# Kernel tuning notes

Hardware: AMD Instinct MI355X
Metric: run time of the kernel (lower is better)

Reference implementation:

```python
import jax, jax.numpy as jnp
import numpy as np

B, Q, K, DQ, DK, H, DV = 4, 512, 512, 512, 512, 256, 512


def setup_inputs() -> dict:
    key = jax.random.key(0)
    ks = jax.random.split(key, 9)
    return {
        "query": jax.random.normal(ks[0], (B, Q, DQ), dtype=jnp.float32),
        "key": jax.random.normal(ks[1], (B, K, DK), dtype=jnp.float32),
        "value": jax.random.normal(ks[2], (B, K, DV), dtype=jnp.float32),
        "Wq": jax.random.normal(ks[3], (DQ, H), dtype=jnp.float32) / np.sqrt(DQ),
        "bq": jax.random.normal(ks[4], (H,), dtype=jnp.float32) * 0.01,
        "Wk": jax.random.normal(ks[5], (DK, H), dtype=jnp.float32) / np.sqrt(DK),
        "bk": jax.random.normal(ks[6], (H,), dtype=jnp.float32) * 0.01,
        "wv": jax.random.normal(ks[7], (H,), dtype=jnp.float32) / np.sqrt(H),
        "bv": jax.random.normal(ks[8], (), dtype=jnp.float32) * 0.01,
    }


def reference(query, key, value, Wq, bq, Wk, bk, wv, bv):
    # Projections: [B,Q,H] and [B,K,H]
    q = jnp.einsum("bqd,dh->bqh", query, Wq) + bq
    k = jnp.einsum("bkd,dh->bkh", key, Wk) + bk
    # Broadcast add + tanh: [B,Q,K,H] (the large intermediate)
    feat = jnp.tanh(q[:, :, None, :] + k[:, None, :, :])
    # Linear-to-scalar score: [B,Q,K]
    score = jnp.einsum("bqkh,h->bqk", feat, wv) + bv
    attention_weight = jax.nn.softmax(score, axis=-1)
    # Dropout is identity at eval; weighted sum over keys: [B,Q,DV]
    context = jnp.einsum("bqk,bkd->bqd", attention_weight, value)
    return (context, attention_weight)
```

## Files before the change

kernel.cpp:

```cpp
#include <hip/hip_runtime.h>
#include <hip/hip_bf16.h>

#define B_ 4
#define Q_ 512
#define K_ 512
#define DQ_ 512
#define H_ 256
#define DV_ 512

#define SC2 2.8853900817779268f

typedef unsigned short u16;
typedef short bf16x8 __attribute__((ext_vector_type(8)));
typedef float f32x4 __attribute__((ext_vector_type(4)));
typedef float f32x2 __attribute__((ext_vector_type(2)));
typedef unsigned short u16x4 __attribute__((ext_vector_type(4)));

__device__ __forceinline__ unsigned bsplit(float a) {
    unsigned u  = __float_as_uint(a);
    unsigned hi = (u + 0x7FFFu + ((u >> 16) & 1u)) >> 16;
    float hf = __uint_as_float(hi << 16);
    float l  = a - hf;
    unsigned ul = __float_as_uint(l);
    unsigned lo = (ul + 0x7FFFu + ((ul >> 16) & 1u)) >> 16;
    return (hi << 16) | lo;
}

__device__ __forceinline__ u16 brn(float a) {
    unsigned u = __float_as_uint(a);
    return (u16)((u + 0x7FFFu + ((u >> 16) & 1u)) >> 16);
}

__device__ __forceinline__ void gld16(const void* g, void* l) {
    __builtin_amdgcn_global_load_lds(
        (const __attribute__((address_space(1))) unsigned int*)g,
        (__attribute__((address_space(3))) unsigned int*)l, 16, 0, 0);
}

__device__ __forceinline__ void pair_acc(
    f32x2 Eq0, f32x2 Eq1, float ek0, float ek1,
    float w0, float w1, float w01, f32x2& acc)
{
    f32x2 e0 = Eq0 * (f32x2){ek0, ek0};
    f32x2 e1 = Eq1 * (f32x2){ek1, ek1};
    f32x2 s  = e0 + e1;
    f32x2 den = __builtin_elementwise_fma(e0, e1, s);
    den = den + (f32x2){1.f, 1.f};
    f32x2 num = __builtin_elementwise_fma(e1, (f32x2){w0, w0}, (f32x2){w01, w01});
    num = __builtin_elementwise_fma(e0, (f32x2){w1, w1}, num);
    f32x2 r = {__builtin_amdgcn_rcpf(den.x), __builtin_amdgcn_rcpf(den.y)};
    acc = __builtin_elementwise_fma(num, r, acc);
}

__global__ __launch_bounds__(256) void prep_all(
    const float* __restrict__ query, const float* __restrict__ key,
    const float* __restrict__ Wq, const float* __restrict__ Wk,
    const float* __restrict__ value,
    u16* __restrict__ qA_hi,
    u16* __restrict__ WT_hi, u16* __restrict__ WT_lo,
    u16* __restrict__ vT_hi)
{
    const int bx  = blockIdx.x;
    const int tid = threadIdx.x;

    if (bx < 2048) {
        const int z = bx >> 10;
        const float* src = z ? key : query;
        u16* dh = qA_hi + (long long)z * 1048576;
        long long i4 = (long long)(bx & 1023) * 256 + tid;
        float4 v = ((const float4*)src)[i4];
        u16x4 h4 = {brn(v.x), brn(v.y), brn(v.z), brn(v.w)};
        *(u16x4*)(dh + i4 * 4) = h4;
        return;
    }

    __shared__ float t[32][33];
    const int flat = bx - 2048;
    const int z  = flat >> 8;
    const int rem = flat & 255;
    const int gx = rem & 15, gy = rem >> 4;
    const int x = tid & 31, y = tid >> 5;
    const float* src; u16 *dh, *dl; int C;
    if (z < 2) {
        if (gy >= 8) return;
        src = z ? Wk : Wq; C = 256;
        dh = WT_hi + (long long)z * 131072;
        dl = WT_lo + (long long)z * 131072;
    } else {
        src = value + (long long)(z - 2) * 262144; C = 512;
        dh = vT_hi + (long long)(z - 2) * 262144;
        dl = nullptr;
    }
    const int r0 = gx * 32, c0 = gy * 32;
    #pragma unroll
    for (int i = 0; i < 32; i += 8)
        t[y + i][x] = src[(long long)(r0 + y + i) * C + c0 + x];
    __syncthreads();
    {
        const int r = tid >> 3, c = tid & 7;
        long long o = (long long)(c0 + r) * 512 + r0 + 4 * c;
        if (dl) {
            unsigned p0 = bsplit(t[4 * c + 0][r]);
            unsigned p1 = bsplit(t[4 * c + 1][r]);
            unsigned p2 = bsplit(t[4 * c + 2][r]);
            unsigned p3 = bsplit(t[4 * c + 3][r]);
            u16x4 h4 = {(u16)(p0 >> 16), (u16)(p1 >> 16), (u16)(p2 >> 16), (u16)(p3 >> 16)};
            u16x4 l4 = {(u16)(p0 & 0xFFFF), (u16)(p1 & 0xFFFF), (u16)(p2 & 0xFFFF), (u16)(p3 & 0xFFFF)};
            *(u16x4*)(dh + o) = h4;
            *(u16x4*)(dl + o) = l4;
        } else {
            u16x4 h4 = {brn(t[4 * c + 0][r]), brn(t[4 * c + 1][r]),
                        brn(t[4 * c + 2][r]), brn(t[4 * c + 3][r])};
            *(u16x4*)(dh + o) = h4;
        }
    }
}

__global__ __launch_bounds__(256) void proj_gemm(
    const u16* __restrict__ Ah0,
    const u16* __restrict__ Bh0, const u16* __restrict__ Bl0,
    const float* __restrict__ biasq, const float* __restrict__ biask,
    float* __restrict__ outp,
    long long sA, long long sB, long long sO)
{
    const int z = blockIdx.z;
    const int Kd = DQ_;
    const u16* Ah = Ah0 + z * sA;
    const u16* Bh = Bh0 + z * sB;
    const u16* Bl = Bl0 + z * sB;

    const int m0 = blockIdx.x * 64;
    const int n0 = blockIdx.y * 64;

    __shared__ u16 AhS[2][64 * 64], BhS[2][64 * 64], BlS[2][64 * 64];

    const int tid = threadIdx.x;
    const int lane = tid & 63, w = tid >> 6;
    const int wr = w >> 1, wc = w & 1;
    const int lrow = lane & 15, lgrp = lane >> 4;

    f32x4 acc[2][2] = {};

    const int idx0 = tid, idx1 = tid + 256;
    const int row0 = idx0 >> 3, u0 = idx0 & 7;
    const int row1 = idx1 >> 3, u1 = idx1 & 7;
    const long long goA0 = (long long)(m0 + row0) * Kd + ((u0 ^ (row0 & 7)) << 3);
    const long long goA1 = (long long)(m0 + row1) * Kd + ((u1 ^ (row1 & 7)) << 3);
    const long long goB0 = (long long)(n0 + row0) * Kd + ((u0 ^ (row0 & 7)) << 3);
    const long long goB1 = (long long)(n0 + row1) * Kd + ((u1 ^ (row1 & 7)) << 3);

#define STAGE(BI, K0) do {                                    \
        gld16(Ah + goA0 + (K0), &AhS[BI][idx0 * 8]);          \
        gld16(Bh + goB0 + (K0), &BhS[BI][idx0 * 8]);          \
        gld16(Bl + goB0 + (K0), &BlS[BI][idx0 * 8]);          \
        gld16(Ah + goA1 + (K0), &AhS[BI][idx1 * 8]);          \
        gld16(Bh + goB1 + (K0), &BhS[BI][idx1 * 8]);          \
        gld16(Bl + goB1 + (K0), &BlS[BI][idx1 * 8]);          \
    } while (0)

    STAGE(0, 0);
    __syncthreads();

    int cur = 0;
    for (int k0 = 0; k0 < Kd; k0 += 64) {
        if (k0 + 64 < Kd) STAGE(cur ^ 1, k0 + 64);

        #pragma unroll
        for (int kk = 0; kk < 2; ++kk) {
            bf16x8 ah[2], bh[2], bl[2];
            #pragma unroll
            for (int f = 0; f < 2; ++f) {
                int ar = wr * 32 + f * 16 + lrow;
                int au = (kk * 4 + lgrp) ^ (ar & 7);
                ah[f] = *(const bf16x8*)(&AhS[cur][ar * 64 + au * 8]);
                int br = wc * 32 + f * 16 + lrow;
                int bu = (kk * 4 + lgrp) ^ (br & 7);
                bh[f] = *(const bf16x8*)(&BhS[cur][br * 64 + bu * 8]);
                bl[f] = *(const bf16x8*)(&BlS[cur][br * 64 + bu * 8]);
            }
            #pragma unroll
            for (int fm = 0; fm < 2; ++fm)
                #pragma unroll
                for (int fn = 0; fn < 2; ++fn) {
                    acc[fm][fn] = __builtin_amdgcn_mfma_f32_16x16x32_bf16(ah[fm], bh[fn], acc[fm][fn], 0, 0, 0);
                    acc[fm][fn] = __builtin_amdgcn_mfma_f32_16x16x32_bf16(ah[fm], bl[fn], acc[fm][fn], 0, 0, 0);
                }
        }
        __syncthreads();
        cur ^= 1;
    }
#undef STAGE

    const float* bs = z ? biask : biasq;
    #pragma unroll
    for (int fm = 0; fm < 2; ++fm)
        #pragma unroll
        for (int fn = 0; fn < 2; ++fn)
            #pragma unroll
            for (int r = 0; r < 4; ++r) {
                int m = m0 + wr * 32 + fm * 16 + lgrp * 4 + r;
                int n = n0 + wc * 32 + fn * 16 + lrow;
                float v = __builtin_amdgcn_exp2f((acc[fm][fn][r] + bs[n]) * SC2);
                if (z == 0) {
                    outp[(((long long)(m >> 2) * H_ + n) << 2) + (m & 3)] = v;
                } else {
                    int bb = m >> 9, k = m & 511;
                    outp[sO + (((long long)(bb * 64 + (n >> 2)) * 512 + k) << 2) + (n & 3)] = v;
                }
            }
}

__global__ __launch_bounds__(256) void pv_gemm(
    const u16* __restrict__ A0, const u16* __restrict__ B0,
    float* __restrict__ ctx)
{
    const int z = blockIdx.z;
    const int Kd = K_;
    const u16* A = A0 + (long long)z * 262144;
    const u16* Bp = B0 + (long long)z * 262144;
    float* C = ctx + (long long)z * 262144;

    const int m0 = blockIdx.x * 64;
    const int n0 = blockIdx.y * 64;

    __shared__ u16 AS[2][64 * 64], BS[2][64 * 64];

    const int tid = threadIdx.x;
    const int lane = tid & 63, w = tid >> 6;
    const int wr = w >> 1, wc = w & 1;
    const int lrow = lane & 15, lgrp = lane >> 4;

    f32x4 acc[2][2] = {};

    const int idx0 = tid, idx1 = tid + 256;
    const int row0 = idx0 >> 3, u0 = idx0 & 7;
    const int row1 = idx1 >> 3, u1 = idx1 & 7;
    const long long goA0 = (long long)(m0 + row0) * Kd + ((u0 ^ (row0 & 7)) << 3);
    const long long goA1 = (long long)(m0 + row1) * Kd + ((u1 ^ (row1 & 7)) << 3);
    const long long goB0 = (long long)(n0 + row0) * Kd + ((u0 ^ (row0 & 7)) << 3);
    const long long goB1 = (long long)(n0 + row1) * Kd + ((u1 ^ (row1 & 7)) << 3);

#define STAGE(BI, K0) do {                                    \
        gld16(A  + goA0 + (K0), &AS[BI][idx0 * 8]);           \
        gld16(Bp + goB0 + (K0), &BS[BI][idx0 * 8]);           \
        gld16(A  + goA1 + (K0), &AS[BI][idx1 * 8]);           \
        gld16(Bp + goB1 + (K0), &BS[BI][idx1 * 8]);           \
    } while (0)

    STAGE(0, 0);
    __syncthreads();

    int cur = 0;
    for (int k0 = 0; k0 < Kd; k0 += 64) {
        if (k0 + 64 < Kd) STAGE(cur ^ 1, k0 + 64);

        #pragma unroll
        for (int kk = 0; kk < 2; ++kk) {
            bf16x8 a[2], b[2];
            #pragma unroll
            for (int f = 0; f < 2; ++f) {
                int ar = wr * 32 + f * 16 + lrow;
                int au = (kk * 4 + lgrp) ^ (ar & 7);
                a[f] = *(const bf16x8*)(&AS[cur][ar * 64 + au * 8]);
                int br = wc * 32 + f * 16 + lrow;
                int bu = (kk * 4 + lgrp) ^ (br & 7);
                b[f] = *(const bf16x8*)(&BS[cur][br * 64 + bu * 8]);
            }
            #pragma unroll
            for (int fm = 0; fm < 2; ++fm)
                #pragma unroll
                for (int fn = 0; fn < 2; ++fn)
                    acc[fm][fn] = __builtin_amdgcn_mfma_f32_16x16x32_bf16(a[fm], b[fn], acc[fm][fn], 0, 0, 0);
        }
        __syncthreads();
        cur ^= 1;
    }
#undef STAGE

    #pragma unroll
    for (int fm = 0; fm < 2; ++fm)
        #pragma unroll
        for (int fn = 0; fn < 2; ++fn)
            #pragma unroll
            for (int r = 0; r < 4; ++r) {
                int m = m0 + wr * 32 + fm * 16 + lgrp * 4 + r;
                int n = n0 + wc * 32 + fn * 16 + lrow;
                C[(long long)m * DV_ + n] = acc[fm][fn][r];
            }
}

#define QT 8

__global__ __launch_bounds__(1024) void score_softmax(
    const float* __restrict__ qp4E,
    const float* __restrict__ kT4E,
    const float* __restrict__ wv,
    float* __restrict__ attn_out,
    u16* __restrict__ aB_hi)
{
    const int b   = blockIdx.y;
    const int q0  = blockIdx.x * QT;
    const int tid = threadIdx.x;
    const int k16 = tid & 255;
    const int qtr = tid >> 8;
    const int lane = tid & 63;

    __shared__ float lq[H_][8];
    __shared__ float lwp[H_ / 2][4];
    __shared__ float pacc[3][2][256][8];
    __shared__ float red[4][QT];

    if (tid < 256) {
        const float4* qA = (const float4*)qp4E + ((long long)(b * (Q_ / 4) + 2 * blockIdx.x)) * H_;
        *(float4*)&lq[tid][0] = qA[tid];
    } else if (tid < 512) {
        int h = tid - 256;
        const float4* qB = (const float4*)qp4E + ((long long)(b * (Q_ / 4) + 2 * blockIdx.x + 1)) * H_;
        *(float4*)&lq[h][4] = qB[h];
    } else if (tid < 512 + 128) {
        int p = tid - 512;
        float w0 = wv[2 * p], w1 = wv[2 * p + 1];
        lwp[p][0] = w0; lwp[p][1] = w1; lwp[p][2] = w0 + w1; lwp[p][3] = 0.f;
    }
    __syncthreads();

    f32x2 aA[4] = {{0.f,0.f},{0.f,0.f},{0.f,0.f},{0.f,0.f}};
    f32x2 aB[4] = {{0.f,0.f},{0.f,0.f},{0.f,0.f},{0.f,0.f}};
    const float4* kvec = (const float4*)kT4E + (long long)b * (H_ / 4) * K_ + k16;
    const int g0 = qtr * 16;

    float4 kA = kvec[(long long)g0 * K_];
    float4 kB = kvec[(long long)g0 * K_ + 256];
    #pragma unroll 2
    for (int gi = 0; gi < 16; ++gi) {
        const int g = g0 + gi;
        float4 kAc = kA, kBc = kB;
        if (gi < 15) {
            kA = kvec[(long long)(g + 1) * K_];
            kB = kvec[(long long)(g + 1) * K_ + 256];
        }
        float4 wp0 = *(const float4*)&lwp[(g << 1) + 0][0];
        float4 wp1 = *(const float4*)&lwp[(g << 1) + 1][0];

        float4 qa0 = *(const float4*)&lq[(g << 2) + 0][0];
        float4 qb0 = *(const float4*)&lq[(g << 2) + 0][4];
        float4 qa1 = *(const float4*)&lq[(g << 2) + 1][0];
        float4 qb1 = *(const float4*)&lq[(g << 2) + 1][4];
        float4 qa2 = *(const float4*)&lq[(g << 2) + 2][0];
        float4 qb2 = *(const float4*)&lq[(g << 2) + 2][4];
        float4 qa3 = *(const float4*)&lq[(g << 2) + 3][0];
        float4 qb3 = *(const float4*)&lq[(g << 2) + 3][4];

        f32x2 q0p[4] = {{qa0.x,qa0.y},{qa0.z,qa0.w},{qb0.x,qb0.y},{qb0.z,qb0.w}};
        f32x2 q1p[4] = {{qa1.x,qa1.y},{qa1.z,qa1.w},{qb1.x,qb1.y},{qb1.z,qb1.w}};
        f32x2 q2p[4] = {{qa2.x,qa2.y},{qa2.z,qa2.w},{qb2.x,qb2.y},{qb2.z,qb2.w}};
        f32x2 q3p[4] = {{qa3.x,qa3.y},{qa3.z,qa3.w},{qb3.x,qb3.y},{qb3.z,qb3.w}};

        #pragma unroll
        for (int qp = 0; qp < 4; ++qp) {
            pair_acc(q0p[qp], q1p[qp], kAc.x, kAc.y, wp0.x, wp0.y, wp0.z, aA[qp]);
            pair_acc(q2p[qp], q3p[qp], kAc.z, kAc.w, wp1.x, wp1.y, wp1.z, aA[qp]);
            pair_acc(q0p[qp], q1p[qp], kBc.x, kBc.y, wp0.x, wp0.y, wp0.z, aB[qp]);
            pair_acc(q2p[qp], q3p[qp], kBc.z, kBc.w, wp1.x, wp1.y, wp1.z, aB[qp]);
        }
    }

    if (qtr) {
        float4 vA0 = make_float4(aA[0].x, aA[0].y, aA[1].x, aA[1].y);
        float4 vA1 = make_float4(aA[2].x, aA[2].y, aA[3].x, aA[3].y);
        float4 vB0 = make_float4(aB[0].x, aB[0].y, aB[1].x, aB[1].y);
        float4 vB1 = make_float4(aB[2].x, aB[2].y, aB[3].x, aB[3].y);
        *(float4*)&pacc[qtr - 1][0][k16][0] = vA0;
        *(float4*)&pacc[qtr - 1][0][k16][4] = vA1;
        *(float4*)&pacc[qtr - 1][1][k16][0] = vB0;
        *(float4*)&pacc[qtr - 1][1][k16][4] = vB1;
    }
    __syncthreads();

    float e[2][QT];
    if (!qtr) {
        float s[2][QT];
        #pragma unroll
        for (int qp = 0; qp < 4; ++qp) {
            s[0][2*qp]   = aA[qp].x;
            s[0][2*qp+1] = aA[qp].y;
            s[1][2*qp]   = aB[qp].x;
            s[1][2*qp+1] = aB[qp].y;
        }
        #pragma unroll
        for (int o = 0; o < 3; ++o) {
            #pragma unroll
            for (int kk = 0; kk < 2; ++kk) {
                float4 t0 = *(const float4*)&pacc[o][kk][k16][0];
                float4 t1 = *(const float4*)&pacc[o][kk][k16][4];
                s[kk][0] += t0.x; s[kk][1] += t0.y; s[kk][2] += t0.z; s[kk][3] += t0.w;
                s[kk][4] += t1.x; s[kk][5] += t1.y; s[kk][6] += t1.z; s[kk][7] += t1.w;
            }
        }
        #pragma unroll
        for (int kk = 0; kk < 2; ++kk)
            #pragma unroll
            for (int qq = 0; qq < QT; ++qq)
                e[kk][qq] = __builtin_amdgcn_exp2f(-SC2 * s[kk][qq]);
        #pragma unroll
        for (int qq = 0; qq < QT; ++qq) {
            float v = e[0][qq] + e[1][qq];
            #pragma unroll
            for (int off = 32; off; off >>= 1) v += __shfl_xor(v, off);
            if (lane == 0) red[tid >> 6][qq] = v;
        }
    }
    __syncthreads();
    if (!qtr) {
        #pragma unroll
        for (int qq = 0; qq < QT; ++qq) {
            float v = red[0][qq] + red[1][qq] + red[2][qq] + red[3][qq];
            float rv = __builtin_amdgcn_rcpf(v);
            #pragma unroll
            for (int kk = 0; kk < 2; ++kk) {
                float a = e[kk][qq] * rv;
                long long o = (long long)(b * Q_ + q0 + qq) * K_ + k16 + kk * 256;
                attn_out[o] = a;
                aB_hi[o] = brn(a);
            }
        }
    }
}

extern "C" void kernel_launch(void* const* d_in, const int* in_sizes, int n_in,
                              void* d_out, int out_size, void* d_ws, size_t ws_size,
                              hipStream_t stream) {
    const float* query = (const float*)d_in[0];
    const float* key   = (const float*)d_in[1];
    const float* value = (const float*)d_in[2];
    const float* Wq    = (const float*)d_in[3];
    const float* bq    = (const float*)d_in[4];
    const float* Wk    = (const float*)d_in[5];
    const float* bk    = (const float*)d_in[6];
    const float* wv    = (const float*)d_in[7];

    float* out = (float*)d_out;
    float* ctx_out  = out;
    float* attn_out = out + (size_t)B_ * Q_ * DV_;

    float* ws   = (float*)d_ws;
    float* qp4  = ws;
    float* kT4  = qp4 + 524288;
    u16* qA_hi  = (u16*)(kT4 + 524288);
    u16* WqT_hi = qA_hi + 2097152;
    u16* WqT_lo = WqT_hi + 262144;
    u16* vT_hi  = WqT_lo + 262144;
    u16* aB_hi  = vT_hi + 1048576;
    (void)n_in; (void)ws_size; (void)in_sizes; (void)out_size;

    hipLaunchKernelGGL(prep_all, dim3(3584), dim3(256), 0, stream,
                       query, key, Wq, Wk, value,
                       qA_hi, WqT_hi, WqT_lo, vT_hi);

    hipLaunchKernelGGL(proj_gemm, dim3(32, 4, 2), dim3(256), 0, stream,
                       qA_hi, WqT_hi, WqT_lo, bq, bk, qp4,
                       (long long)1048576, (long long)131072, (long long)524288);

    hipLaunchKernelGGL(score_softmax, dim3(Q_ / QT, B_), dim3(1024), 0, stream,
                       qp4, kT4, wv, attn_out, aB_hi);

    hipLaunchKernelGGL(pv_gemm, dim3(8, 8, 4), dim3(256), 0, stream,
                       aB_hi, vT_hi, ctx_out);
}
```

Before: 60.33 us.

## Fuse all four stages into one persistent kernel with grid barriers

Replaces the four separate launches (prep, projection GEMM, score/softmax, PV GEMM) with a single 256-block persistent kernel of 1024 threads. The stages are separated by software grid-wide barriers built on atomic counters, and a memset clears the counters before launch. This removes per-launch overhead and the drain and fill gaps between kernels. In exchange the tiling changes to one 16x16 MFMA tile per wave with 1024-thread blocks, which may lower per-stage efficiency. The spin barriers also depend on all 256 blocks being resident at once, otherwise the kernel deadlocks.

```diff
diff --git a/kernel.cpp b/kernel.cpp
--- a/kernel.cpp
+++ b/kernel.cpp
@@ -52,377 +52,353 @@
     acc = __builtin_elementwise_fma(num, r, acc);
 }
 
-__global__ __launch_bounds__(256) void prep_all(
-    const float* __restrict__ query, const float* __restrict__ key,
-    const float* __restrict__ Wq, const float* __restrict__ Wk,
-    const float* __restrict__ value,
-    u16* __restrict__ qA_hi,
-    u16* __restrict__ WT_hi, u16* __restrict__ WT_lo,
-    u16* __restrict__ vT_hi)
-{
-    const int bx  = blockIdx.x;
-    const int tid = threadIdx.x;
-
-    if (bx < 2048) {
-        const int z = bx >> 10;
-        const float* src = z ? key : query;
-        u16* dh = qA_hi + (long long)z * 1048576;
-        long long i4 = (long long)(bx & 1023) * 256 + tid;
-        float4 v = ((const float4*)src)[i4];
-        u16x4 h4 = {brn(v.x), brn(v.y), brn(v.z), brn(v.w)};
-        *(u16x4*)(dh + i4 * 4) = h4;
-        return;
-    }
-
-    __shared__ float t[32][33];
-    const int flat = bx - 2048;
-    const int z  = flat >> 8;
-    const int rem = flat & 255;
-    const int gx = rem & 15, gy = rem >> 4;
-    const int x = tid & 31, y = tid >> 5;
-    const float* src; u16 *dh, *dl; int C;
-    if (z < 2) {
-        if (gy >= 8) return;
-        src = z ? Wk : Wq; C = 256;
-        dh = WT_hi + (long long)z * 131072;
-        dl = WT_lo + (long long)z * 131072;
-    } else {
-        src = value + (long long)(z - 2) * 262144; C = 512;
-        dh = vT_hi + (long long)(z - 2) * 262144;
-        dl = nullptr;
-    }
-    const int r0 = gx * 32, c0 = gy * 32;
-    #pragma unroll
-    for (int i = 0; i < 32; i += 8)
-        t[y + i][x] = src[(long long)(r0 + y + i) * C + c0 + x];
+__device__ __forceinline__ void gsync(unsigned* syncp, int slot) {
     __syncthreads();
-    {
-        const int r = tid >> 3, c = tid & 7;
-        long long o = (long long)(c0 + r) * 512 + r0 + 4 * c;
-        if (dl) {
-            unsigned p0 = bsplit(t[4 * c + 0][r]);
-            unsigned p1 = bsplit(t[4 * c + 1][r]);
-            unsigned p2 = bsplit(t[4 * c + 2][r]);
-            unsigned p3 = bsplit(t[4 * c + 3][r]);
-            u16x4 h4 = {(u16)(p0 >> 16), (u16)(p1 >> 16), (u16)(p2 >> 16), (u16)(p3 >> 16)};
-            u16x4 l4 = {(u16)(p0 & 0xFFFF), (u16)(p1 & 0xFFFF), (u16)(p2 & 0xFFFF), (u16)(p3 & 0xFFFF)};
-            *(u16x4*)(dh + o) = h4;
-            *(u16x4*)(dl + o) = l4;
+    if (threadIdx.x == 0) {
+        unsigned* cnt  = syncp + slot * 32;
+        unsigned* flag = syncp + slot * 32 + 16;
+        __threadfence();
+        unsigned prev = atomicAdd(cnt, 1u);
+        if (prev == gridDim.x - 1) {
+            atomicExch(flag, 1u);
         } else {
-            u16x4 h4 = {brn(t[4 * c + 0][r]), brn(t[4 * c + 1][r]),
-                        brn(t[4 * c + 2][r]), brn(t[4 * c + 3][r])};
-            *(u16x4*)(dh + o) = h4;
-        }
-    }
-}
-
-__global__ __launch_bounds__(256) void proj_gemm(
-    const u16* __restrict__ Ah0,
-    const u16* __restrict__ Bh0, const u16* __restrict__ Bl0,
-    const float* __restrict__ biasq, const float* __restrict__ biask,
-    float* __restrict__ outp,
-    long long sA, long long sB, long long sO)
-{
-    const int z = blockIdx.z;
-    const int Kd = DQ_;
-    const u16* Ah = Ah0 + z * sA;
-    const u16* Bh = Bh0 + z * sB;
-    const u16* Bl = Bl0 + z * sB;
-
-    const int m0 = blockIdx.x * 64;
-    const int n0 = blockIdx.y * 64;
-
-    __shared__ u16 AhS[2][64 * 64], BhS[2][64 * 64], BlS[2][64 * 64];
-
-    const int tid = threadIdx.x;
-    const int lane = tid & 63, w = tid >> 6;
-    const int wr = w >> 1, wc = w & 1;
-    const int lrow = lane & 15, lgrp = lane >> 4;
-
-    f32x4 acc[2][2] = {};
-
-    const int idx0 = tid, idx1 = tid + 256;
-    const int row0 = idx0 >> 3, u0 = idx0 & 7;
-    const int row1 = idx1 >> 3, u1 = idx1 & 7;
-    const long long goA0 = (long long)(m0 + row0) * Kd + ((u0 ^ (row0 & 7)) << 3);
-    const long long goA1 = (long long)(m0 + row1) * Kd + ((u1 ^ (row1 & 7)) << 3);
-    const long long goB0 = (long long)(n0 + row0) * Kd + ((u0 ^ (row0 & 7)) << 3);
-    const long long goB1 = (long long)(n0 + row1) * Kd + ((u1 ^ (row1 & 7)) << 3);
-
-#define STAGE(BI, K0) do {                                    \
-        gld16(Ah + goA0 + (K0), &AhS[BI][idx0 * 8]);          \
-        gld16(Bh + goB0 + (K0), &BhS[BI][idx0 * 8]);          \
-        gld16(Bl + goB0 + (K0), &BlS[BI][idx0 * 8]);          \
-        gld16(Ah + goA1 + (K0), &AhS[BI][idx1 * 8]);          \
-        gld16(Bh + goB1 + (K0), &BhS[BI][idx1 * 8]);          \
-        gld16(Bl + goB1 + (K0), &BlS[BI][idx1 * 8]);          \
-    } while (0)
-
-    STAGE(0, 0);
-    __syncthreads();
-
-    int cur = 0;
-    for (int k0 = 0; k0 < Kd; k0 += 64) {
-        if (k0 + 64 < Kd) STAGE(cur ^ 1, k0 + 64);
-
-        #pragma unroll
-        for (int kk = 0; kk < 2; ++kk) {
-            bf16x8 ah[2], bh[2], bl[2];
-            #pragma unroll
-            for (int f = 0; f < 2; ++f) {
-                int ar = wr * 32 + f * 16 + lrow;
-                int au = (kk * 4 + lgrp) ^ (ar & 7);
-                ah[f] = *(const bf16x8*)(&AhS[cur][ar * 64 + au * 8]);
-                int br = wc * 32 + f * 16 + lrow;
-                int bu = (kk * 4 + lgrp) ^ (br & 7);
-                bh[f] = *(const bf16x8*)(&BhS[cur][br * 64 + bu * 8]);
-                bl[f] = *(const bf16x8*)(&BlS[cur][br * 64 + bu * 8]);
-            }
-            #pragma unroll
-            for (int fm = 0; fm < 2; ++fm)
-                #pragma unroll
-                for (int fn = 0; fn < 2; ++fn) {
-                    acc[fm][fn] = __builtin_amdgcn_mfma_f32_16x16x32_bf16(ah[fm], bh[fn], acc[fm][fn], 0, 0, 0);
-                    acc[fm][fn] = __builtin_amdgcn_mfma_f32_16x16x32_bf16(ah[fm], bl[fn], acc[fm][fn], 0, 0, 0);
-                }
-        }
-        __syncthreads();
-        cur ^= 1;
-    }
-#undef STAGE
-
-    const float* bs = z ? biask : biasq;
-    #pragma unroll
-    for (int fm = 0; fm < 2; ++fm)
-        #pragma unroll
-        for (int fn = 0; fn < 2; ++fn)
-            #pragma unroll
-            for (int r = 0; r < 4; ++r) {
-                int m = m0 + wr * 32 + fm * 16 + lgrp * 4 + r;
-                int n = n0 + wc * 32 + fn * 16 + lrow;
-                float v = __builtin_amdgcn_exp2f((acc[fm][fn][r] + bs[n]) * SC2);
-                if (z == 0) {
-                    outp[(((long long)(m >> 2) * H_ + n) << 2) + (m & 3)] = v;
-                } else {
-                    int bb = m >> 9, k = m & 511;
-                    outp[sO + (((long long)(bb * 64 + (n >> 2)) * 512 + k) << 2) + (n & 3)] = v;
-                }
-            }
-}
-
-__global__ __launch_bounds__(256) void pv_gemm(
-    const u16* __restrict__ A0, const u16* __restrict__ B0,
-    float* __restrict__ ctx)
-{
-    const int z = blockIdx.z;
-    const int Kd = K_;
-    const u16* A = A0 + (long long)z * 262144;
-    const u16* Bp = B0 + (long long)z * 262144;
-    float* C = ctx + (long long)z * 262144;
-
-    const int m0 = blockIdx.x * 64;
-    const int n0 = blockIdx.y * 64;
-
-    __shared__ u16 AS[2][64 * 64], BS[2][64 * 64];
-
-    const int tid = threadIdx.x;
-    const int lane = tid & 63, w = tid >> 6;
-    const int wr = w >> 1, wc = w & 1;
-    const int lrow = lane & 15, lgrp = lane >> 4;
-
-    f32x4 acc[2][2] = {};
-
-    const int idx0 = tid, idx1 = tid + 256;
-    const int row0 = idx0 >> 3, u0 = idx0 & 7;
-    const int row1 = idx1 >> 3, u1 = idx1 & 7;
-    const long long goA0 = (long long)(m0 + row0) * Kd + ((u0 ^ (row0 & 7)) << 3);
-    const long long goA1 = (long long)(m0 + row1) * Kd + ((u1 ^ (row1 & 7)) << 3);
-    const long long goB0 = (long long)(n0 + row0) * Kd + ((u0 ^ (row0 & 7)) << 3);
-    const long long goB1 = (long long)(n0 + row1) * Kd + ((u1 ^ (row1 & 7)) << 3);
-
-#define STAGE(BI, K0) do {                                    \
-        gld16(A  + goA0 + (K0), &AS[BI][idx0 * 8]);           \
-        gld16(Bp + goB0 + (K0), &BS[BI][idx0 * 8]);           \
-        gld16(A  + goA1 + (K0), &AS[BI][idx1 * 8]);           \
-        gld16(Bp + goB1 + (K0), &BS[BI][idx1 * 8]);           \
-    } while (0)
-
-    STAGE(0, 0);
-    __syncthreads();
-
-    int cur = 0;
-    for (int k0 = 0; k0 < Kd; k0 += 64) {
-        if (k0 + 64 < Kd) STAGE(cur ^ 1, k0 + 64);
-
-        #pragma unroll
-        for (int kk = 0; kk < 2; ++kk) {
-            bf16x8 a[2], b[2];
-            #pragma unroll
-            for (int f = 0; f < 2; ++f) {
-                int ar = wr * 32 + f * 16 + lrow;
-                int au = (kk * 4 + lgrp) ^ (ar & 7);
-                a[f] = *(const bf16x8*)(&AS[cur][ar * 64 + au * 8]);
-                int br = wc * 32 + f * 16 + lrow;
-                int bu = (kk * 4 + lgrp) ^ (br & 7);
-                b[f] = *(const bf16x8*)(&BS[cur][br * 64 + bu * 8]);
-            }
-            #pragma unroll
-            for (int fm = 0; fm < 2; ++fm)
-                #pragma unroll
-                for (int fn = 0; fn < 2; ++fn)
-                    acc[fm][fn] = __builtin_amdgcn_mfma_f32_16x16x32_bf16(a[fm], b[fn], acc[fm][fn], 0, 0, 0);
-        }
-        __syncthreads();
-        cur ^= 1;
-    }
-#undef STAGE
-
-    #pragma unroll
-    for (int fm = 0; fm < 2; ++fm)
-        #pragma unroll
-        for (int fn = 0; fn < 2; ++fn)
-            #pragma unroll
-            for (int r = 0; r < 4; ++r) {
-                int m = m0 + wr * 32 + fm * 16 + lgrp * 4 + r;
-                int n = n0 + wc * 32 + fn * 16 + lrow;
-                C[(long long)m * DV_ + n] = acc[fm][fn][r];
-            }
-}
-
-#define QT 8
-
-__global__ __launch_bounds__(1024) void score_softmax(
-    const float* __restrict__ qp4E,
-    const float* __restrict__ kT4E,
-    const float* __restrict__ wv,
-    float* __restrict__ attn_out,
-    u16* __restrict__ aB_hi)
-{
-    const int b   = blockIdx.y;
-    const int q0  = blockIdx.x * QT;
-    const int tid = threadIdx.x;
-    const int k16 = tid & 255;
-    const int qtr = tid >> 8;
-    const int lane = tid & 63;
-
-    __shared__ float lq[H_][8];
-    __shared__ float lwp[H_ / 2][4];
-    __shared__ float pacc[3][2][256][8];
-    __shared__ float red[4][QT];
-
-    if (tid < 256) {
-        const float4* qA = (const float4*)qp4E + ((long long)(b * (Q_ / 4) + 2 * blockIdx.x)) * H_;
-        *(float4*)&lq[tid][0] = qA[tid];
-    } else if (tid < 512) {
-        int h = tid - 256;
-        const float4* qB = (const float4*)qp4E + ((long long)(b * (Q_ / 4) + 2 * blockIdx.x + 1)) * H_;
-        *(float4*)&lq[h][4] = qB[h];
-    } else if (tid < 512 + 128) {
-        int p = tid - 512;
-        float w0 = wv[2 * p], w1 = wv[2 * p + 1];
-        lwp[p][0] = w0; lwp[p][1] = w1; lwp[p][2] = w0 + w1; lwp[p][3] = 0.f;
+            while (atomicAdd(flag, 0u) == 0u) __builtin_amdgcn_s_sleep(2);
+        }
+        __threadfence();
     }
     __syncthreads();
-
-    f32x2 aA[4] = {{0.f,0.f},{0.f,0.f},{0.f,0.f},{0.f,0.f}};
-    f32x2 aB[4] = {{0.f,0.f},{0.f,0.f},{0.f,0.f},{0.f,0.f}};
-    const float4* kvec = (const float4*)kT4E + (long long)b * (H_ / 4) * K_ + k16;
-    const int g0 = qtr * 16;
-
-    float4 kA = kvec[(long long)g0 * K_];
-    float4 kB = kvec[(long long)g0 * K_ + 256];
-    #pragma unroll 2
-    for (int gi = 0; gi < 16; ++gi) {
-        const int g = g0 + gi;
-        float4 kAc = kA, kBc = kB;
-        if (gi < 15) {
-            kA = kvec[(long long)(g + 1) * K_];
-            kB = kvec[(long long)(g + 1) * K_ + 256];
-        }
-        float4 wp0 = *(const float4*)&lwp[(g << 1) + 0][0];
-        float4 wp1 = *(const float4*)&lwp[(g << 1) + 1][0];
-
-        float4 qa0 = *(const float4*)&lq[(g << 2) + 0][0];
-        float4 qb0 = *(const float4*)&lq[(g << 2) + 0][4];
-        float4 qa1 = *(const float4*)&lq[(g << 2) + 1][0];
-        float4 qb1 = *(const float4*)&lq[(g << 2) + 1][4];
-        float4 qa2 = *(const float4*)&lq[(g << 2) + 2][0];
-        float4 qb2 = *(const float4*)&lq[(g << 2) + 2][4];
-        float4 qa3 = *(const float4*)&lq[(g << 2) + 3][0];
-        float4 qb3 = *(const float4*)&lq[(g << 2) + 3][4];
-
-        f32x2 q0p[4] = {{qa0.x,qa0.y},{qa0.z,qa0.w},{qb0.x,qb0.y},{qb0.z,qb0.w}};
-        f32x2 q1p[4] = {{qa1.x,qa1.y},{qa1.z,qa1.w},{qb1.x,qb1.y},{qb1.z,qb1.w}};
-        f32x2 q2p[4] = {{qa2.x,qa2.y},{qa2.z,qa2.w},{qb2.x,qb2.y},{qb2.z,qb2.w}};
-        f32x2 q3p[4] = {{qa3.x,qa3.y},{qa3.z,qa3.w},{qb3.x,qb3.y},{qb3.z,qb3.w}};
-
+}
+
+#define QT 8
+
+__global__ __launch_bounds__(1024) void fused_all(
+    const float* __restrict__ query, const float* __restrict__ key,
+    const float* __restrict__ value,
+    const float* __restrict__ Wq, const float* __restrict__ bq,
+    const float* __restrict__ Wk, const float* __restrict__ bk,
+    const float* __restrict__ wv,
+    float* __restrict__ ctx_out, float* __restrict__ attn_out,
+    unsigned* __restrict__ syncp,
+    float* __restrict__ qp4E, float* __restrict__ kT4E,
+    u16* __restrict__ qA_hi, u16* __restrict__ WT_hi, u16* __restrict__ WT_lo,
+    u16* __restrict__ vT_hi, u16* __restrict__ aB_hi)
+{
+    __shared__ __align__(16) unsigned char smem[61440];
+    const int tid = threadIdx.x;
+    const int bid = blockIdx.x;
+    const int lane = tid & 63;
+    const int lrow = lane & 15, lgrp = lane >> 4;
+
+    {
+        int gid = bid * 1024 + tid;
+        float4 vq = ((const float4*)query)[gid];
+        float4 vk = ((const float4*)key)[gid];
+        u16x4 hq = {brn(vq.x), brn(vq.y), brn(vq.z), brn(vq.w)};
+        u16x4 hk = {brn(vk.x), brn(vk.y), brn(vk.z), brn(vk.w)};
+        *(u16x4*)(qA_hi + (long long)gid * 4) = hq;
+        *(u16x4*)(qA_hi + 1048576 + (long long)gid * 4) = hk;
+
+        const int grp = tid >> 8, lt = tid & 255;
+        const int x = lt & 31, y = lt >> 5;
+        float (*tg)[33] = (float(*)[33])(smem + grp * 4224);
         #pragma unroll
-        for (int qp = 0; qp < 4; ++qp) {
-            pair_acc(q0p[qp], q1p[qp], kAc.x, kAc.y, wp0.x, wp0.y, wp0.z, aA[qp]);
-            pair_acc(q2p[qp], q3p[qp], kAc.z, kAc.w, wp1.x, wp1.y, wp1.z, aA[qp]);
-            pair_acc(q0p[qp], q1p[qp], kBc.x, kBc.y, wp0.x, wp0.y, wp0.z, aB[qp]);
-            pair_acc(q2p[qp], q3p[qp], kBc.z, kBc.w, wp1.x, wp1.y, wp1.z, aB[qp]);
+        for (int rnd = 0; rnd < 2; ++rnd) {
+            int tidc = bid * 8 + grp * 2 + rnd;
+            bool act = tidc < 1280;
+            const float* src = query; u16 *dh = nullptr, *dl = nullptr;
+            int C = 512, r0 = 0, c0 = 0;
+            if (act) {
+                int z, gx, gy;
+                if (tidc < 256) {
+                    z = tidc >> 7; int r2 = tidc & 127; gx = r2 & 15; gy = r2 >> 4;
+                    src = z ? Wk : Wq; C = 256;
+                    dh = WT_hi + (long long)z * 131072;
+                    dl = WT_lo + (long long)z * 131072;
+                } else {
+                    int t = tidc - 256; z = t >> 8; int rem = t & 255;
+                    gx = rem & 15; gy = rem >> 4;
+                    src = value + (long long)z * 262144; C = 512;
+                    dh = vT_hi + (long long)z * 262144;
+                    dl = nullptr;
+                }
+                r0 = gx * 32; c0 = gy * 32;
+                #pragma unroll
+                for (int i = 0; i < 32; i += 8)
+                    tg[y + i][x] = src[(long long)(r0 + y + i) * C + c0 + x];
+            }
+            __syncthreads();
+            if (act) {
+                const int r = lt >> 3, c = lt & 7;
+                long long o = (long long)(c0 + r) * 512 + r0 + 4 * c;
+                if (dl) {
+                    unsigned p0 = bsplit(tg[4 * c + 0][r]);
+                    unsigned p1 = bsplit(tg[4 * c + 1][r]);
+                    unsigned p2 = bsplit(tg[4 * c + 2][r]);
+                    unsigned p3 = bsplit(tg[4 * c + 3][r]);
+                    u16x4 h4 = {(u16)(p0 >> 16), (u16)(p1 >> 16), (u16)(p2 >> 16), (u16)(p3 >> 16)};
+                    u16x4 l4 = {(u16)(p0 & 0xFFFF), (u16)(p1 & 0xFFFF), (u16)(p2 & 0xFFFF), (u16)(p3 & 0xFFFF)};
+                    *(u16x4*)(dh + o) = h4;
+                    *(u16x4*)(dl + o) = l4;
+                } else {
+                    u16x4 h4 = {brn(tg[4 * c + 0][r]), brn(tg[4 * c + 1][r]),
+                                brn(tg[4 * c + 2][r]), brn(tg[4 * c + 3][r])};
+                    *(u16x4*)(dh + o) = h4;
+                }
+            }
+            __syncthreads();
         }
     }
-
-    if (qtr) {
-        float4 vA0 = make_float4(aA[0].x, aA[0].y, aA[1].x, aA[1].y);
-        float4 vA1 = make_float4(aA[2].x, aA[2].y, aA[3].x, aA[3].y);
-        float4 vB0 = make_float4(aB[0].x, aB[0].y, aB[1].x, aB[1].y);
-        float4 vB1 = make_float4(aB[2].x, aB[2].y, aB[3].x, aB[3].y);
-        *(float4*)&pacc[qtr - 1][0][k16][0] = vA0;
-        *(float4*)&pacc[qtr - 1][0][k16][4] = vA1;
-        *(float4*)&pacc[qtr - 1][1][k16][0] = vB0;
-        *(float4*)&pacc[qtr - 1][1][k16][4] = vB1;
+    gsync(syncp, 0);
+
+    {
+        u16* AhS = (u16*)smem;
+        u16* BhS = AhS + 8192;
+        u16* BlS = AhS + 16384;
+        const int wv16 = tid >> 6;
+        const int fr = (wv16 >> 2) * 16, fc = (wv16 & 3) * 16;
+        const int stg = tid & 511;
+        const int rowS = stg >> 3, uS = stg & 7;
+        const long long swz = (long long)((uS ^ (rowS & 7)) << 3);
+
+        const int z  = bid & 1;
+        const int n0 = ((bid >> 1) & 3) * 64;
+        const int m0 = (bid >> 3) * 64;
+        const u16* Ah = qA_hi + (long long)z * 1048576;
+        const u16* Bh = WT_hi + (long long)z * 131072;
+        const u16* Bl = WT_lo + (long long)z * 131072;
+        const long long goA = (long long)(m0 + rowS) * 512 + swz;
+        const long long goB = (long long)(n0 + rowS) * 512 + swz;
+
+        f32x4 acc = {0.f, 0.f, 0.f, 0.f};
+
+#define PSTAGE(BI, K0) do {                                           \
+        if (tid < 512) {                                              \
+            gld16(Ah + goA + (K0), AhS + (BI) * 4096 + stg * 8);      \
+            gld16(Bl + goB + (K0), BlS + (BI) * 4096 + stg * 8);      \
+        } else {                                                      \
+            gld16(Bh + goB + (K0), BhS + (BI) * 4096 + stg * 8);      \
+        }                                                             \
+    } while (0)
+
+        PSTAGE(0, 0);
+        __syncthreads();
+        int cur = 0;
+        for (int k0 = 0; k0 < DQ_; k0 += 64) {
+            if (k0 + 64 < DQ_) PSTAGE(cur ^ 1, k0 + 64);
+            #pragma unroll
+            for (int kk = 0; kk < 2; ++kk) {
+                int ar = fr + lrow;
+                int au = (kk * 4 + lgrp) ^ (ar & 7);
+                bf16x8 a = *(const bf16x8*)(AhS + cur * 4096 + ar * 64 + au * 8);
+                int br = fc + lrow;
+                int bu = (kk * 4 + lgrp) ^ (br & 7);
+                bf16x8 bh = *(const bf16x8*)(BhS + cur * 4096 + br * 64 + bu * 8);
+                bf16x8 bl = *(const bf16x8*)(BlS + cur * 4096 + br * 64 + bu * 8);
+                acc = __builtin_amdgcn_mfma_f32_16x16x32_bf16(a, bh, acc, 0, 0, 0);
+                acc = __builtin_amdgcn_mfma_f32_16x16x32_bf16(a, bl, acc, 0, 0, 0);
+            }
+            __syncthreads();
+            cur ^= 1;
+        }
+#undef PSTAGE
+
+        const float* bs = z ? bk : bq;
+        #pragma unroll
+        for (int r = 0; r < 4; ++r) {
+            int m = m0 + fr + lgrp * 4 + r;
+            int n = n0 + fc + lrow;
+            float v = __builtin_amdgcn_exp2f((acc[r] + bs[n]) * SC2);
+            if (z == 0) {
+                qp4E[(((long long)(m >> 2) * H_ + n) << 2) + (m & 3)] = v;
+            } else {
+                int bb = m >> 9, k = m & 511;
+                kT4E[(((long long)(bb * 64 + (n >> 2)) * 512 + k) << 2) + (n & 3)] = v;
+            }
+        }
     }
-    __syncthreads();
-
-    float e[2][QT];
-    if (!qtr) {
-        float s[2][QT];
+    gsync(syncp, 1);
+
+    {
+        const int bx = bid & 63;
+        const int b  = bid >> 6;
+        const int q0 = bx * QT;
+        const int k16 = tid & 255;
+        const int qtr = tid >> 8;
+
+        float (*lq)[8]   = (float(*)[8])smem;
+        float (*lwp)[4]  = (float(*)[4])(smem + 8192);
+        float (*red)[QT] = (float(*)[QT])(smem + 10240);
+        float (*pacc)[2][256][8] = (float(*)[2][256][8])(smem + 12288);
+
+        if (tid < 256) {
+            const float4* qA = (const float4*)qp4E + ((long long)(b * (Q_ / 4) + 2 * bx)) * H_;
+            *(float4*)&lq[tid][0] = qA[tid];
+        } else if (tid < 512) {
+            int h = tid - 256;
+            const float4* qB = (const float4*)qp4E + ((long long)(b * (Q_ / 4) + 2 * bx + 1)) * H_;
+            *(float4*)&lq[h][4] = qB[h];
+        } else if (tid < 512 + 128) {
+            int p = tid - 512;
+            float w0 = wv[2 * p], w1 = wv[2 * p + 1];
+            lwp[p][0] = w0; lwp[p][1] = w1; lwp[p][2] = w0 + w1; lwp[p][3] = 0.f;
+        }
+        __syncthreads();
+
+        f32x2 aA[4] = {{0.f,0.f},{0.f,0.f},{0.f,0.f},{0.f,0.f}};
+        f32x2 aB[4] = {{0.f,0.f},{0.f,0.f},{0.f,0.f},{0.f,0.f}};
+        const float4* kvec = (const float4*)kT4E + (long long)b * (H_ / 4) * K_ + k16;
+        const int g0 = qtr * 16;
+
+        float4 kA = kvec[(long long)g0 * K_];
+        float4 kB = kvec[(long long)g0 * K_ + 256];
+        #pragma unroll 2
+        for (int gi = 0; gi < 16; ++gi) {
+            const int g = g0 + gi;
+            float4 kAc = kA, kBc = kB;
+            if (gi < 15) {
+                kA = kvec[(long long)(g + 1) * K_];
+                kB = kvec[(long long)(g + 1) * K_ + 256];
+            }
+            float4 wp0 = *(const float4*)&lwp[(g << 1) + 0][0];
+            float4 wp1 = *(const float4*)&lwp[(g << 1) + 1][0];
+
+            float4 qa0 = *(const float4*)&lq[(g << 2) + 0][0];
+            float4 qb0 = *(const float4*)&lq[(g << 2) + 0][4];
+            float4 qa1 = *(const float4*)&lq[(g << 2) + 1][0];
+            float4 qb1 = *(const float4*)&lq[(g << 2) + 1][4];
+            float4 qa2 = *(const float4*)&lq[(g << 2) + 2][0];
+            float4 qb2 = *(const float4*)&lq[(g << 2) + 2][4];
+            float4 qa3 = *(const float4*)&lq[(g << 2) + 3][0];
+            float4 qb3 = *(const float4*)&lq[(g << 2) + 3][4];
+
+            f32x2 q0p[4] = {{qa0.x,qa0.y},{qa0.z,qa0.w},{qb0.x,qb0.y},{qb0.z,qb0.w}};
+            f32x2 q1p[4] = {{qa1.x,qa1.y},{qa1.z,qa1.w},{qb1.x,qb1.y},{qb1.z,qb1.w}};
+            f32x2 q2p[4] = {{qa2.x,qa2.y},{qa2.z,qa2.w},{qb2.x,qb2.y},{qb2.z,qb2.w}};
+            f32x2 q3p[4] = {{qa3.x,qa3.y},{qa3.z,qa3.w},{qb3.x,qb3.y},{qb3.z,qb3.w}};
+
+            #pragma unroll
+            for (int qp = 0; qp < 4; ++qp) {
+                pair_acc(q0p[qp], q1p[qp], kAc.x, kAc.y, wp0.x, wp0.y, wp0.z, aA[qp]);
+                pair_acc(q2p[qp], q3p[qp], kAc.z, kAc.w, wp1.x, wp1.y, wp1.z, aA[qp]);
+                pair_acc(q0p[qp], q1p[qp], kBc.x, kBc.y, wp0.x, wp0.y, wp0.z, aB[qp]);
+                pair_acc(q2p[qp], q3p[qp], kBc.z, kBc.w, wp1.x, wp1.y, wp1.z, aB[qp]);
+            }
+        }
+
+        if (qtr) {
+            float4 vA0 = make_float4(aA[0].x, aA[0].y, aA[1].x, aA[1].y);
+            float4 vA1 = make_float4(aA[2].x, aA[2].y, aA[3].x, aA[3].y);
+            float4 vB0 = make_float4(aB[0].x, aB[0].y, aB[1].x, aB[1].y);
+            float4 vB1 = make_float4(aB[2].x, aB[2].y, aB[3].x, aB[3].y);
+            *(float4*)&pacc[qtr - 1][0][k16][0] = vA0;
+            *(float4*)&pacc[qtr - 1][0][k16][4] = vA1;
+            *(float4*)&pacc[qtr - 1][1][k16][0] = vB0;
+            *(float4*)&pacc[qtr - 1][1][k16][4] = vB1;
+        }
+        __syncthreads();
+
+        float e[2][QT];
+        if (!qtr) {
+            float s[2][QT];
+            #pragma unroll
+            for (int qp = 0; qp < 4; ++qp) {
+                s[0][2*qp]   = aA[qp].x;
+                s[0][2*qp+1] = aA[qp].y;
+                s[1][2*qp]   = aB[qp].x;
+                s[1][2*qp+1] = aB[qp].y;
+            }
+            #pragma unroll
+            for (int o = 0; o < 3; ++o) {
+                #pragma unroll
+                for (int kk = 0; kk < 2; ++kk) {
+                    float4 t0 = *(const float4*)&pacc[o][kk][k16][0];
+                    float4 t1 = *(const float4*)&pacc[o][kk][k16][4];
+                    s[kk][0] += t0.x; s[kk][1] += t0.y; s[kk][2] += t0.z; s[kk][3] += t0.w;
+                    s[kk][4] += t1.x; s[kk][5] += t1.y; s[kk][6] += t1.z; s[kk][7] += t1.w;
+                }
+            }
+            #pragma unroll
+            for (int kk = 0; kk < 2; ++kk)
+                #pragma unroll
+                for (int qq = 0; qq < QT; ++qq)
+                    e[kk][qq] = __builtin_amdgcn_exp2f(-SC2 * s[kk][qq]);
+            #pragma unroll
+            for (int qq = 0; qq < QT; ++qq) {
+                float v = e[0][qq] + e[1][qq];
+                #pragma unroll
+                for (int off = 32; off; off >>= 1) v += __shfl_xor(v, off);
+                if (lane == 0) red[tid >> 6][qq] = v;
+            }
+        }
+        __syncthreads();
+        if (!qtr) {
+            #pragma unroll
+            for (int qq = 0; qq < QT; ++qq) {
+                float v = red[0][qq] + red[1][qq] + red[2][qq] + red[3][qq];
+                float rv = __builtin_amdgcn_rcpf(v);
+                #pragma unroll
+                for (int kk = 0; kk < 2; ++kk) {
+                    float a = e[kk][qq] * rv;
+                    long long o = (long long)(b * Q_ + q0 + qq) * K_ + k16 + kk * 256;
+                    attn_out[o] = a;
+                    aB_hi[o] = brn(a);
+                }
+            }
+        }
+        __syncthreads();
+    }
+    gsync(syncp, 2);
+
+    {
+        u16* AS = (u16*)smem;
+        u16* BS = AS + 8192;
+        const int z  = bid >> 6;
+        const int n0 = ((bid >> 3) & 7) * 64;
+        const int m0 = (bid & 7) * 64;
+        const u16* A  = aB_hi + (long long)z * 262144;
+        const u16* Bp = vT_hi + (long long)z * 262144;
+        float* C = ctx_out + (long long)z * 262144;
+
+        const int wv16 = tid >> 6;
+        const int fr = (wv16 >> 2) * 16, fc = (wv16 & 3) * 16;
+        const int stg = tid & 511;
+        const int rowS = stg >> 3, uS = stg & 7;
+        const long long swz = (long long)((uS ^ (rowS & 7)) << 3);
+        const long long goA = (long long)(m0 + rowS) * 512 + swz;
+        const long long goB = (long long)(n0 + rowS) * 512 + swz;
+
+        f32x4 acc = {0.f, 0.f, 0.f, 0.f};
+
+#define VSTAGE(BI, K0) do {                                          \
+        if (tid < 512) gld16(A  + goA + (K0), AS + (BI) * 4096 + stg * 8); \
+        else           gld16(Bp + goB + (K0), BS + (BI) * 4096 + stg * 8); \
+    } while (0)
+
+        VSTAGE(0, 0);
+        __syncthreads();
+        int cur = 0;
+        for (int k0 = 0; k0 < K_; k0 += 64) {
+            if (k0 + 64 < K_) VSTAGE(cur ^ 1, k0 + 64);
+            #pragma unroll
+            for (int kk = 0; kk < 2; ++kk) {
+                int ar = fr + lrow;
+                int au = (kk * 4 + lgrp) ^ (ar & 7);
+                bf16x8 a = *(const bf16x8*)(AS + cur * 4096 + ar * 64 + au * 8);
+                int br = fc + lrow;
+                int bu = (kk * 4 + lgrp) ^ (br & 7);
+                bf16x8 b = *(const bf16x8*)(BS + cur * 4096 + br * 64 + bu * 8);
+                acc = __builtin_amdgcn_mfma_f32_16x16x32_bf16(a, b, acc, 0, 0, 0);
+            }
+            __syncthreads();
+            cur ^= 1;
+        }
+#undef VSTAGE
+
         #pragma unroll
-        for (int qp = 0; qp < 4; ++qp) {
-            s[0][2*qp]   = aA[qp].x;
-            s[0][2*qp+1] = aA[qp].y;
-            s[1][2*qp]   = aB[qp].x;
-            s[1][2*qp+1] = aB[qp].y;
-        }
-        #pragma unroll
-        for (int o = 0; o < 3; ++o) {
-            #pragma unroll
-            for (int kk = 0; kk < 2; ++kk) {
-                float4 t0 = *(const float4*)&pacc[o][kk][k16][0];
-                float4 t1 = *(const float4*)&pacc[o][kk][k16][4];
-                s[kk][0] += t0.x; s[kk][1] += t0.y; s[kk][2] += t0.z; s[kk][3] += t0.w;
-                s[kk][4] += t1.x; s[kk][5] += t1.y; s[kk][6] += t1.z; s[kk][7] += t1.w;
-            }
-        }
-        #pragma unroll
-        for (int kk = 0; kk < 2; ++kk)
-            #pragma unroll
-            for (int qq = 0; qq < QT; ++qq)
-                e[kk][qq] = __builtin_amdgcn_exp2f(-SC2 * s[kk][qq]);
-        #pragma unroll
-        for (int qq = 0; qq < QT; ++qq) {
-            float v = e[0][qq] + e[1][qq];
-            #pragma unroll
-            for (int off = 32; off; off >>= 1) v += __shfl_xor(v, off);
-            if (lane == 0) red[tid >> 6][qq] = v;
-        }
-    }
-    __syncthreads();
-    if (!qtr) {
-        #pragma unroll
-        for (int qq = 0; qq < QT; ++qq) {
-            float v = red[0][qq] + red[1][qq] + red[2][qq] + red[3][qq];
-            float rv = __builtin_amdgcn_rcpf(v);
-            #pragma unroll
-            for (int kk = 0; kk < 2; ++kk) {
-                float a = e[kk][qq] * rv;
-                long long o = (long long)(b * Q_ + q0 + qq) * K_ + k16 + kk * 256;
-                attn_out[o] = a;
-                aB_hi[o] = brn(a);
-            }
+        for (int r = 0; r < 4; ++r) {
+            int m = m0 + fr + lgrp * 4 + r;
+            int n = n0 + fc + lrow;
+            C[(long long)m * DV_ + n] = acc[r];
         }
     }
 }
@@ -443,27 +419,20 @@
     float* ctx_out  = out;
     float* attn_out = out + (size_t)B_ * Q_ * DV_;
 
-    float* ws   = (float*)d_ws;
-    float* qp4  = ws;
+    unsigned* syncp = (unsigned*)d_ws;
+    float* qp4  = (float*)d_ws + 256;
     float* kT4  = qp4 + 524288;
     u16* qA_hi  = (u16*)(kT4 + 524288);
-    u16* WqT_hi = qA_hi + 2097152;
-    u16* WqT_lo = WqT_hi + 262144;
-    u16* vT_hi  = WqT_lo + 262144;
+    u16* WT_hi  = qA_hi + 2097152;
+    u16* WT_lo  = WT_hi + 262144;
+    u16* vT_hi  = WT_lo + 262144;
     u16* aB_hi  = vT_hi + 1048576;
     (void)n_in; (void)ws_size; (void)in_sizes; (void)out_size;
 
-    hipLaunchKernelGGL(prep_all, dim3(3584), dim3(256), 0, stream,
-                       query, key, Wq, Wk, value,
-                       qA_hi, WqT_hi, WqT_lo, vT_hi);
-
-    hipLaunchKernelGGL(proj_gemm, dim3(32, 4, 2), dim3(256), 0, stream,
-                       qA_hi, WqT_hi, WqT_lo, bq, bk, qp4,
-                       (long long)1048576, (long long)131072, (long long)524288);
-
-    hipLaunchKernelGGL(score_softmax, dim3(Q_ / QT, B_), dim3(1024), 0, stream,
-                       qp4, kT4, wv, attn_out, aB_hi);
-
-    hipLaunchKernelGGL(pv_gemm, dim3(8, 8, 4), dim3(256), 0, stream,
-                       aB_hi, vT_hi, ctx_out);
-}
+    hipMemsetAsync(d_ws, 0, 1024, stream);
+
+    hipLaunchKernelGGL(fused_all, dim3(256), dim3(1024), 0, stream,
+                       query, key, value, Wq, bq, Wk, bk, wv,
+                       ctx_out, attn_out, syncp,
+                       qp4, kT4, qA_hi, WT_hi, WT_lo, vT_hi, aB_hi);
+}
```

After: 132.2 us. 2.19x slower.
